# Performance work log

Hardware: AMD Instinct MI355X
Metric: run time of the kernel (lower is better)

## Reference

```python
import jax, jax.numpy as jnp
import numpy as np

TEMPERATURE = 0.5
EPS = 1e-8  # torch CosineSimilarity default eps


def setup_inputs() -> dict:
    key = jax.random.key(0)
    k1, k2 = jax.random.split(key)
    N, D = 4096, 256
    return {
        "batch_embeddings": jax.random.normal(k1, (N, D), dtype=jnp.float32),
        "batch_augmented_embeddings": jax.random.normal(k2, (N, D), dtype=jnp.float32),
    }


def reference(batch_embeddings, batch_augmented_embeddings):
    N = batch_embeddings.shape[0]
    emb = jnp.concatenate([batch_embeddings, batch_augmented_embeddings], axis=0)  # (2N, D)
    # cosine similarity = normalized dot products (normalize + GEMM rewrite of the
    # broadcasted nn.CosineSimilarity)
    norms = jnp.sqrt(jnp.sum(emb * emb, axis=-1, keepdims=True))
    emb_n = emb / jnp.maximum(norms, EPS)
    sim = jnp.einsum("id,jd->ij", emb_n, emb_n) / TEMPERATURE  # (2N, 2N)
    # negative mask: (~eye(N)).repeat(2,2) -> False where (i mod N) == (j mod N)
    idx = jnp.arange(2 * N)
    neg_mask = (idx[:, None] % N) != (idx[None, :] % N)
    exp_sim = jnp.exp(sim) * neg_mask.astype(sim.dtype)
    sum_exp = jnp.sum(exp_sim, axis=-1)  # (2N,)
    pos = jnp.arange(N)
    positive_sim = sim[pos, N + pos]  # (N,)
    negative_sim_sum = sum_exp[:N]  # (N,)
    loss = -jnp.mean(jnp.log(jnp.exp(positive_sim) / negative_sim_sum))
    return loss
```

## Files before the change

### kernel.cpp

```cpp
#include <hip/hip_runtime.h>
#include <hip/hip_bf16.h>

#define NROWS 4096
#define DDIM  256
#define EPS   1e-8f
#define SCALE 1.69864944f
#define LN2   0.69314718056f

#define NJ    32
#define JS    256
#define BT    32
#define LSTRIDE 264

typedef __attribute__((ext_vector_type(8))) short short8;
typedef __attribute__((ext_vector_type(4))) float f32x4;

#if __has_builtin(__builtin_amdgcn_exp2f)
#define EXP2F(x) __builtin_amdgcn_exp2f(x)
#else
#define EXP2F(x) exp2f(x)
#endif

__global__ void normalize_kernel(const float* __restrict__ a,
                                 const float* __restrict__ b,
                                 __hip_bfloat16* __restrict__ en,
                                 float* __restrict__ S, int N) {
    const int row = blockIdx.x;
    const int t = threadIdx.x;
    const float* src = (row < N) ? (a + (size_t)row * DDIM)
                                 : (b + (size_t)(row - N) * DDIM);
    float x = src[t];
    float ss = x * x;
    #pragma unroll
    for (int off = 32; off > 0; off >>= 1) ss += __shfl_xor(ss, off);
    __shared__ float wsum[4];
    const int wave = t >> 6, lane = t & 63;
    if (lane == 0) wsum[wave] = ss;
    __syncthreads();
    const float tot = wsum[0] + wsum[1] + wsum[2] + wsum[3];
    const float inv = SCALE / fmaxf(sqrtf(tot), EPS);
    en[(size_t)row * DDIM + t] = __float2bfloat16(x * inv);
    if (t == 0 && row < N) S[row] = 0.0f;
}

__global__ __launch_bounds__(256) void simsum_kernel(
        const short* __restrict__ en,
        float* __restrict__ S,
        float* __restrict__ pos) {
    __shared__ short bt[BT * LSTRIDE];
    const int tid = threadIdx.x;
    const int wave = tid >> 6, lane = tid & 63;
    const int lrow = lane & 15, quad = lane >> 4;
    const int i0 = blockIdx.x * 256 + wave * 64;

    short8 afrag[4][8];
    #pragma unroll
    for (int t = 0; t < 4; ++t) {
        #pragma unroll
        for (int ks = 0; ks < 8; ++ks) {
            afrag[t][ks] = *reinterpret_cast<const short8*>(
                en + (size_t)(i0 + t * 16 + lrow) * DDIM + ks * 32 + quad * 8);
        }
    }

    float rowsum[4][4];
    #pragma unroll
    for (int t = 0; t < 4; ++t)
        #pragma unroll
        for (int r = 0; r < 4; ++r) rowsum[t][r] = 0.0f;

    const int jb = blockIdx.y * JS;
    for (int jc = jb; jc < jb + JS; jc += BT) {
        __syncthreads();
        const short* src = en + (size_t)jc * DDIM;
        #pragma unroll
        for (int it = 0; it < 4; ++it) {
            const int off = it * 2048 + tid * 8;
            short8 v = *reinterpret_cast<const short8*>(src + off);
            *reinterpret_cast<short8*>(
                &bt[(off >> 8) * LSTRIDE + (off & 255)]) = v;
        }
        __syncthreads();

        #pragma unroll
        for (int c = 0; c < 2; ++c) {
            f32x4 acc[4];
            #pragma unroll
            for (int t = 0; t < 4; ++t) acc[t] = f32x4{0.f, 0.f, 0.f, 0.f};
            #pragma unroll
            for (int ks = 0; ks < 8; ++ks) {
                short8 bfrag = *reinterpret_cast<const short8*>(
                    &bt[(c * 16 + lrow) * LSTRIDE + ks * 32 + quad * 8]);
                #pragma unroll
                for (int t = 0; t < 4; ++t) {
                    acc[t] = __builtin_amdgcn_mfma_f32_16x16x32_bf16(
                        afrag[t][ks], bfrag, acc[t], 0, 0, 0);
                }
            }
            const int col = jc + c * 16 + lrow;
            const int cm = col & (NROWS - 1);
            #pragma unroll
            for (int t = 0; t < 4; ++t) {
                const int rbase = i0 + t * 16 + quad * 4;
                #pragma unroll
                for (int r = 0; r < 4; ++r) {
                    const float d = acc[t][r];
                    const int row = rbase + r;
                    rowsum[t][r] += (cm != row) ? EXP2F(d) : 0.0f;
                    if (cm == row && col >= NROWS)
                        pos[row] = d * LN2;
                }
            }
        }
    }

    #pragma unroll
    for (int t = 0; t < 4; ++t) {
        #pragma unroll
        for (int r = 0; r < 4; ++r) {
            float v = rowsum[t][r];
            v += __shfl_xor(v, 1);
            v += __shfl_xor(v, 2);
            v += __shfl_xor(v, 4);
            v += __shfl_xor(v, 8);
            rowsum[t][r] = v;
        }
        if (lrow < 4) {
            const float v = (lrow == 0) ? rowsum[t][0]
                          : (lrow == 1) ? rowsum[t][1]
                          : (lrow == 2) ? rowsum[t][2]
                          :               rowsum[t][3];
            atomicAdd(&S[i0 + t * 16 + quad * 4 + lrow], v);
        }
    }
}

__global__ void loss_kernel(const float* __restrict__ S,
                            const float* __restrict__ pos,
                            float* __restrict__ out, int N) {
    float acc = 0.0f;
    for (int i = threadIdx.x; i < N; i += blockDim.x)
        acc += pos[i] - __logf(S[i]);
    #pragma unroll
    for (int off = 32; off > 0; off >>= 1) acc += __shfl_xor(acc, off);
    __shared__ float wsum[4];
    const int wave = threadIdx.x >> 6, lane = threadIdx.x & 63;
    if (lane == 0) wsum[wave] = acc;
    __syncthreads();
    if (threadIdx.x == 0)
        out[0] = -(wsum[0] + wsum[1] + wsum[2] + wsum[3]) / (float)N;
}

extern "C" void kernel_launch(void* const* d_in, const int* in_sizes, int n_in,
                              void* d_out, int out_size, void* d_ws, size_t ws_size,
                              hipStream_t stream) {
    const float* a = (const float*)d_in[0];
    const float* b = (const float*)d_in[1];
    float* out = (float*)d_out;
    const int N = NROWS;

    char* ws = (char*)d_ws;
    __hip_bfloat16* en = (__hip_bfloat16*)ws;
    float* S = (float*)(ws + (size_t)2 * N * DDIM * sizeof(__hip_bfloat16));
    float* pos = S + N;

    normalize_kernel<<<2 * N, 256, 0, stream>>>(a, b, en, S, N);
    simsum_kernel<<<dim3(N / 256, NJ), 256, 0, stream>>>((const short*)en, S, pos);
    loss_kernel<<<1, 256, 0, stream>>>(S, pos, out, N);
}
```

Baseline: 96.67 us.

## Double-buffer B tiles via direct global-to-LDS loads and restructure normalize

The similarity kernel now stages 64-column B tiles straight into LDS with global_load_lds into two alternating buffers, so the next tile loads while MFMAs run on the current one. It also drops one barrier per chunk and moves the diagonal mask out of the inner loop: every exp is added, and the diagonal term is subtracted afterwards. The normalize kernel now processes one row per wave with float4 loads and no shared-memory reduction, and the loss kernel uses 1024 threads. The subtract-after-add diagonal handling can introduce small rounding differences, and the LDS layout relies on global_load_lds write ordering being correct.

```diff
diff --git a/kernel.cpp b/kernel.cpp
--- a/kernel.cpp
+++ b/kernel.cpp
@@ -7,10 +7,11 @@
 #define SCALE 1.69864944f
 #define LN2   0.69314718056f
 
-#define NJ    32
-#define JS    256
-#define BT    32
-#define LSTRIDE 264
+#define NJ 32
+#define JS 256
+#define BT 64
+#define CH (JS / BT)
+#define BUFSH (4 * 8 * 64 * 8)
 
 typedef __attribute__((ext_vector_type(8))) short short8;
 typedef __attribute__((ext_vector_type(4))) float f32x4;
@@ -21,47 +22,52 @@
 #define EXP2F(x) exp2f(x)
 #endif
 
+__device__ __forceinline__ unsigned short f2bf(float x) {
+    union { __hip_bfloat16 h; unsigned short u; } c;
+    c.h = __float2bfloat16(x);
+    return c.u;
+}
+
 __global__ void normalize_kernel(const float* __restrict__ a,
                                  const float* __restrict__ b,
-                                 __hip_bfloat16* __restrict__ en,
+                                 unsigned short* __restrict__ en,
                                  float* __restrict__ S, int N) {
-    const int row = blockIdx.x;
-    const int t = threadIdx.x;
+    const int wave = threadIdx.x >> 6, lane = threadIdx.x & 63;
+    const int row = blockIdx.x * 4 + wave;
     const float* src = (row < N) ? (a + (size_t)row * DDIM)
                                  : (b + (size_t)(row - N) * DDIM);
-    float x = src[t];
-    float ss = x * x;
+    const float4 v = reinterpret_cast<const float4*>(src)[lane];
+    float ss = v.x * v.x + v.y * v.y + v.z * v.z + v.w * v.w;
     #pragma unroll
     for (int off = 32; off > 0; off >>= 1) ss += __shfl_xor(ss, off);
-    __shared__ float wsum[4];
-    const int wave = t >> 6, lane = t & 63;
-    if (lane == 0) wsum[wave] = ss;
-    __syncthreads();
-    const float tot = wsum[0] + wsum[1] + wsum[2] + wsum[3];
-    const float inv = SCALE / fmaxf(sqrtf(tot), EPS);
-    en[(size_t)row * DDIM + t] = __float2bfloat16(x * inv);
-    if (t == 0 && row < N) S[row] = 0.0f;
+    const float inv = SCALE / fmaxf(sqrtf(ss), EPS * SCALE);
+    ushort4 o;
+    o.x = f2bf(v.x * inv);
+    o.y = f2bf(v.y * inv);
+    o.z = f2bf(v.z * inv);
+    o.w = f2bf(v.w * inv);
+    *reinterpret_cast<ushort4*>(en + (size_t)row * DDIM + lane * 4) = o;
+    if (lane == 0 && row < N) S[row] = 0.0f;
 }
 
-__global__ __launch_bounds__(256) void simsum_kernel(
+__global__ __launch_bounds__(256, 2) void simsum_kernel(
         const short* __restrict__ en,
         float* __restrict__ S,
         float* __restrict__ pos) {
-    __shared__ short bt[BT * LSTRIDE];
+    __shared__ short bt[2 * BUFSH];
     const int tid = threadIdx.x;
     const int wave = tid >> 6, lane = tid & 63;
     const int lrow = lane & 15, quad = lane >> 4;
     const int i0 = blockIdx.x * 256 + wave * 64;
+    const int jb = blockIdx.y * JS;
 
     short8 afrag[4][8];
     #pragma unroll
-    for (int t = 0; t < 4; ++t) {
+    for (int t = 0; t < 4; ++t)
         #pragma unroll
-        for (int ks = 0; ks < 8; ++ks) {
+        for (int ks = 0; ks < 8; ++ks)
             afrag[t][ks] = *reinterpret_cast<const short8*>(
                 en + (size_t)(i0 + t * 16 + lrow) * DDIM + ks * 32 + quad * 8);
-        }
-    }
 
     float rowsum[4][4];
     #pragma unroll
@@ -69,46 +75,55 @@
         #pragma unroll
         for (int r = 0; r < 4; ++r) rowsum[t][r] = 0.0f;
 
-    const int jb = blockIdx.y * JS;
-    for (int jc = jb; jc < jb + JS; jc += BT) {
+    auto stage = [&](int jc, int buf) {
+        const short* g = en + (size_t)(jc + wave * 16 + lrow) * DDIM + quad * 8;
+        short* l = bt + buf * BUFSH + wave * 4096;
+        #pragma unroll
+        for (int ks = 0; ks < 8; ++ks) {
+            __builtin_amdgcn_global_load_lds(
+                (const __attribute__((address_space(1))) void*)(g + ks * 32),
+                (__attribute__((address_space(3))) void*)(l + ks * 512),
+                16, 0, 0);
+        }
+    };
+
+    stage(jb, 0);
+    for (int c = 0; c < CH; ++c) {
         __syncthreads();
-        const short* src = en + (size_t)jc * DDIM;
+        if (c + 1 < CH) stage(jb + (c + 1) * BT, (c + 1) & 1);
+        const short* lb = bt + (c & 1) * BUFSH;
         #pragma unroll
-        for (int it = 0; it < 4; ++it) {
-            const int off = it * 2048 + tid * 8;
-            short8 v = *reinterpret_cast<const short8*>(src + off);
-            *reinterpret_cast<short8*>(
-                &bt[(off >> 8) * LSTRIDE + (off & 255)]) = v;
-        }
-        __syncthreads();
-
-        #pragma unroll
-        for (int c = 0; c < 2; ++c) {
+        for (int cg = 0; cg < 4; ++cg) {
             f32x4 acc[4];
             #pragma unroll
             for (int t = 0; t < 4; ++t) acc[t] = f32x4{0.f, 0.f, 0.f, 0.f};
             #pragma unroll
             for (int ks = 0; ks < 8; ++ks) {
-                short8 bfrag = *reinterpret_cast<const short8*>(
-                    &bt[(c * 16 + lrow) * LSTRIDE + ks * 32 + quad * 8]);
+                const short8 bfrag = *reinterpret_cast<const short8*>(
+                    lb + cg * 4096 + ks * 512 + lane * 8);
                 #pragma unroll
-                for (int t = 0; t < 4; ++t) {
+                for (int t = 0; t < 4; ++t)
                     acc[t] = __builtin_amdgcn_mfma_f32_16x16x32_bf16(
                         afrag[t][ks], bfrag, acc[t], 0, 0, 0);
-                }
             }
-            const int col = jc + c * 16 + lrow;
+            const int col = jb + c * BT + cg * 16 + lrow;
             const int cm = col & (NROWS - 1);
             #pragma unroll
             for (int t = 0; t < 4; ++t) {
-                const int rbase = i0 + t * 16 + quad * 4;
                 #pragma unroll
-                for (int r = 0; r < 4; ++r) {
-                    const float d = acc[t][r];
-                    const int row = rbase + r;
-                    rowsum[t][r] += (cm != row) ? EXP2F(d) : 0.0f;
-                    if (cm == row && col >= NROWS)
-                        pos[row] = d * LN2;
+                for (int r = 0; r < 4; ++r)
+                    rowsum[t][r] += EXP2F(acc[t][r]);
+                const unsigned delta = (unsigned)(cm - (i0 + t * 16 + quad * 4));
+                if (delta < 4u) {
+                    const float d = (delta == 0) ? acc[t][0]
+                                  : (delta == 1) ? acc[t][1]
+                                  : (delta == 2) ? acc[t][2]
+                                  :                acc[t][3];
+                    const float ed = EXP2F(d);
+                    #pragma unroll
+                    for (int r = 0; r < 4; ++r)
+                        if (r == (int)delta) rowsum[t][r] -= ed;
+                    if (col >= NROWS) pos[cm] = d * LN2;
                 }
             }
         }
@@ -139,16 +154,20 @@
                             const float* __restrict__ pos,
                             float* __restrict__ out, int N) {
     float acc = 0.0f;
-    for (int i = threadIdx.x; i < N; i += blockDim.x)
+    for (int i = threadIdx.x; i < N; i += 1024)
         acc += pos[i] - __logf(S[i]);
     #pragma unroll
     for (int off = 32; off > 0; off >>= 1) acc += __shfl_xor(acc, off);
-    __shared__ float wsum[4];
+    __shared__ float wsum[16];
     const int wave = threadIdx.x >> 6, lane = threadIdx.x & 63;
     if (lane == 0) wsum[wave] = acc;
     __syncthreads();
-    if (threadIdx.x == 0)
-        out[0] = -(wsum[0] + wsum[1] + wsum[2] + wsum[3]) / (float)N;
+    if (threadIdx.x == 0) {
+        float tot = 0.0f;
+        #pragma unroll
+        for (int w = 0; w < 16; ++w) tot += wsum[w];
+        out[0] = -tot / (float)N;
+    }
 }
 
 extern "C" void kernel_launch(void* const* d_in, const int* in_sizes, int n_in,
@@ -160,11 +179,11 @@
     const int N = NROWS;
 
     char* ws = (char*)d_ws;
-    __hip_bfloat16* en = (__hip_bfloat16*)ws;
-    float* S = (float*)(ws + (size_t)2 * N * DDIM * sizeof(__hip_bfloat16));
+    unsigned short* en = (unsigned short*)ws;
+    float* S = (float*)(ws + (size_t)2 * N * DDIM * sizeof(unsigned short));
     float* pos = S + N;
 
-    normalize_kernel<<<2 * N, 256, 0, stream>>>(a, b, en, S, N);
+    normalize_kernel<<<(2 * N) / 4, 256, 0, stream>>>(a, b, en, S, N);
     simsum_kernel<<<dim3(N / 256, NJ), 256, 0, stream>>>((const short*)en, S, pos);
-    loss_kernel<<<1, 256, 0, stream>>>(S, pos, out, N);
+    loss_kernel<<<1, 1024, 0, stream>>>(S, pos, out, N);
 }
```

Measured after the change: 88.48 us. 1.09x faster.
